# Kernel tuning notes

Measured on AMD Instinct MI355X. Metric: run time of the kernel, lower is better.

Reference implementation:

```python
import jax, jax.numpy as jnp
import numpy as np

N_EMBED = 768
N_HEAD = 12
HEAD = N_EMBED // N_HEAD
B, T = 4, 2048


def setup_inputs() -> dict:
    key = jax.random.key(0)
    ks = jax.random.split(key, 12)
    s = 0.02
    d = N_EMBED
    return {
        "x": jax.random.normal(ks[0], (B, T, d), jnp.float32),
        "ln1_g": jnp.ones((d,), jnp.float32),
        "ln1_b": jnp.zeros((d,), jnp.float32),
        "w_attn": jax.random.normal(ks[1], (d, 3 * d), jnp.float32) * s,
        "b_attn": jnp.zeros((3 * d,), jnp.float32),
        "w_aproj": jax.random.normal(ks[2], (d, d), jnp.float32) * s,
        "b_aproj": jnp.zeros((d,), jnp.float32),
        "ln2_g": jnp.ones((d,), jnp.float32),
        "ln2_b": jnp.zeros((d,), jnp.float32),
        "w_fc": jax.random.normal(ks[3], (d, 4 * d), jnp.float32) * s,
        "b_fc": jnp.zeros((4 * d,), jnp.float32),
        "w_mproj": jax.random.normal(ks[4], (4 * d, d), jnp.float32) * s,
        "b_mproj": jnp.zeros((d,), jnp.float32),
    }


def _layernorm(x, g, b, eps=1e-5):
    mu = jnp.mean(x, axis=-1, keepdims=True)
    var = jnp.var(x, axis=-1, keepdims=True)
    return (x - mu) * jax.lax.rsqrt(var + eps) * g + b


def _attn(x, w_attn, b_attn, w_aproj, b_aproj):
    Bq, Tq, C = x.shape
    qkv = x @ w_attn + b_attn  # [B,T,3C]
    q, k, v = jnp.split(qkv, 3, axis=2)
    q = q.reshape(Bq, Tq, N_HEAD, HEAD).transpose(0, 2, 1, 3)  # [B,H,T,hd]
    k = k.reshape(Bq, Tq, N_HEAD, HEAD).transpose(0, 2, 1, 3)
    v = v.reshape(Bq, Tq, N_HEAD, HEAD).transpose(0, 2, 1, 3)
    att = jnp.einsum("bhqd,bhkd->bhqk", q, k) * (1.0 / np.sqrt(HEAD))
    causal = jnp.tril(jnp.ones((Tq, Tq), bool))
    att = jnp.where(causal, att, -jnp.inf)
    att = jax.nn.softmax(att, axis=-1)
    y = jnp.einsum("bhqk,bhkd->bhqd", att, v)
    y = y.transpose(0, 2, 1, 3).reshape(Bq, Tq, C)
    return y @ w_aproj + b_aproj


def reference(x, ln1_g, ln1_b, w_attn, b_attn, w_aproj, b_aproj,
              ln2_g, ln2_b, w_fc, b_fc, w_mproj, b_mproj):
    x = x + _attn(_layernorm(x, ln1_g, ln1_b), w_attn, b_attn, w_aproj, b_aproj)
    h = _layernorm(x, ln2_g, ln2_b)
    h = jax.nn.gelu(h @ w_fc + b_fc, approximate=False)
    x = x + (h @ w_mproj + b_mproj)
    return x
```

## Files before the change

### kernel.cpp

```cpp
#include <hip/hip_runtime.h>
#include <hip/hip_bf16.h>

#define NE 768
#define NH 12
#define HD 64
#define BB 4
#define TT 2048
#define ROWS (BB*TT)

typedef __attribute__((ext_vector_type(8))) short bf16x8;
typedef __attribute__((ext_vector_type(4))) float f32x4;

#define WAITV(N) asm volatile("s_waitcnt vmcnt(" #N ")" ::: "memory")
#define BARSYNC()                                   \
  do {                                              \
    __builtin_amdgcn_sched_barrier(0);              \
    __builtin_amdgcn_s_barrier();                   \
    __builtin_amdgcn_sched_barrier(0);              \
  } while (0)

__device__ __forceinline__ short f2bf(float f) {
  __hip_bfloat16 h = __float2bfloat16(f);
  union { __hip_bfloat16 h; short s; } u; u.h = h; return u.s;
}

__device__ __forceinline__ void gload16(const void* g, void* l) {
  __builtin_amdgcn_global_load_lds(
      (const __attribute__((address_space(1))) void*)g,
      (__attribute__((address_space(3))) void*)l,
      16, 0, 0);
}

__device__ __forceinline__ void xcd_remap(int id, int nbn, int& bm, int& bn) {
  int x = id & 7;
  int j = id >> 3;
  bm = x * 8 + j / nbn;
  bn = j % nbn;
}

__global__ __launch_bounds__(256) void wtrans_kernel(
    const float* __restrict__ W, short* __restrict__ Wt, int K, int N) {
  __shared__ short tile[64 * 65];
  int k0 = blockIdx.x * 64, n0 = blockIdx.y * 64;
  int t = threadIdx.x;
#pragma unroll
  for (int p = 0; p < 16; ++p) {
    int idx = p * 256 + t;
    int r = idx >> 6, c = idx & 63;
    tile[r * 65 + c] = f2bf(W[(size_t)(k0 + r) * N + n0 + c]);
  }
  __syncthreads();
#pragma unroll
  for (int p = 0; p < 16; ++p) {
    int idx = p * 256 + t;
    int rr = idx >> 6, cc = idx & 63;
    Wt[(size_t)(n0 + rr) * K + k0 + cc] = tile[cc * 65 + rr];
  }
}

__global__ __launch_bounds__(256) void vtrans_kernel(
    const short* __restrict__ qkv, short* __restrict__ vt) {
  __shared__ short tile[64 * 65];
  int bh = blockIdx.x;
  int b = bh / NH, h = bh % NH;
  int t0 = blockIdx.y * 64;
  int t = threadIdx.x;
#pragma unroll
  for (int p = 0; p < 16; ++p) {
    int idx = p * 256 + t;
    int r = idx >> 6, c = idx & 63;
    tile[r * 65 + c] =
        qkv[(size_t)(b * TT + t0 + r) * (3 * NE) + 2 * NE + h * HD + c];
  }
  __syncthreads();
#pragma unroll
  for (int p = 0; p < 16; ++p) {
    int idx = p * 256 + t;
    int rr = idx >> 6, cc = idx & 63;
    vt[(size_t)bh * HD * TT + (size_t)rr * TT + t0 + cc] = tile[cc * 65 + rr];
  }
}

__global__ __launch_bounds__(64) void ln_kernel(
    const float* __restrict__ x, const float* __restrict__ g,
    const float* __restrict__ b, short* __restrict__ out) {
  int row = blockIdx.x, l = threadIdx.x;
  const float* xr = x + (size_t)row * NE;
  float4 v[3];
  float s = 0.f, ss = 0.f;
#pragma unroll
  for (int i = 0; i < 3; ++i) {
    v[i] = *reinterpret_cast<const float4*>(xr + l * 4 + i * 256);
    s += v[i].x + v[i].y + v[i].z + v[i].w;
    ss += v[i].x * v[i].x + v[i].y * v[i].y + v[i].z * v[i].z + v[i].w * v[i].w;
  }
#pragma unroll
  for (int m = 1; m < 64; m <<= 1) {
    s += __shfl_xor(s, m);
    ss += __shfl_xor(ss, m);
  }
  float mu = s * (1.0f / NE);
  float var = ss * (1.0f / NE) - mu * mu;
  float rstd = rsqrtf(var + 1e-5f);
#pragma unroll
  for (int i = 0; i < 3; ++i) {
    float4 gv = *reinterpret_cast<const float4*>(g + l * 4 + i * 256);
    float4 bv = *reinterpret_cast<const float4*>(b + l * 4 + i * 256);
    short4 o;
    o.x = f2bf((v[i].x - mu) * rstd * gv.x + bv.x);
    o.y = f2bf((v[i].y - mu) * rstd * gv.y + bv.y);
    o.z = f2bf((v[i].z - mu) * rstd * gv.z + bv.z);
    o.w = f2bf((v[i].w - mu) * rstd * gv.w + bv.w);
    *reinterpret_cast<short4*>(out + (size_t)row * NE + l * 4 + i * 256) = o;
  }
}

template <int EPI>
__global__ __launch_bounds__(256) void gemm_kernel(
    const short* __restrict__ A, const short* __restrict__ Bt,
    const float* __restrict__ bias, const float* __restrict__ resid,
    void* __restrict__ Cout, int M, int N, int K, int nbn) {
  __shared__ short As[3][128 * 32];
  __shared__ short Bs[3][128 * 32];
  int t = threadIdx.x;
  int w = t >> 6, l = t & 63;
  int wr = w >> 1, wc = w & 1;
  int bm, bn;
  xcd_remap(blockIdx.x, nbn, bm, bn);
  int lr = l & 15, g4 = l >> 4;

  f32x4 acc[4][4];
#pragma unroll
  for (int i = 0; i < 4; ++i)
#pragma unroll
    for (int j = 0; j < 4; ++j) acc[i][j] = (f32x4){0.f, 0.f, 0.f, 0.f};

  int r0 = t >> 2;
  int cs = ((t & 3) ^ (r0 & 3)) * 8;
  const short* ga = A + (size_t)(bm * 128) * K;
  const short* gb = Bt + (size_t)(bn * 128) * K;

#pragma unroll
  for (int p = 0; p < 2; ++p) {
    int ko = p * 32;
    gload16(ga + (size_t)r0 * K + ko + cs, &As[p][t * 8]);
    gload16(ga + (size_t)(r0 + 64) * K + ko + cs, &As[p][(t + 256) * 8]);
    gload16(gb + (size_t)r0 * K + ko + cs, &Bs[p][t * 8]);
    gload16(gb + (size_t)(r0 + 64) * K + ko + cs, &Bs[p][(t + 256) * 8]);
  }

  int xorA = (lr & 3) << 4;
  int nk = K >> 5;
  int cur = 0, prv = 2;
  for (int kt = 0; kt < nk; ++kt) {
    if (kt < nk - 1) WAITV(4); else WAITV(0);
    BARSYNC();
    if (kt + 2 < nk) {
      int ko = (kt + 2) * 32;
      gload16(ga + (size_t)r0 * K + ko + cs, &As[prv][t * 8]);
      gload16(ga + (size_t)(r0 + 64) * K + ko + cs, &As[prv][(t + 256) * 8]);
      gload16(gb + (size_t)r0 * K + ko + cs, &Bs[prv][t * 8]);
      gload16(gb + (size_t)(r0 + 64) * K + ko + cs, &Bs[prv][(t + 256) * 8]);
    }
    __builtin_amdgcn_sched_barrier(0);
    const char* Ab = (const char*)As[cur];
    const char* Bb = (const char*)Bs[cur];
    bf16x8 af[4], bfr[4];
#pragma unroll
    for (int i = 0; i < 4; ++i)
      af[i] = *reinterpret_cast<const bf16x8*>(
          Ab + (((wr * 64 + i * 16 + lr) * 64 + g4 * 16) ^ xorA));
#pragma unroll
    for (int j = 0; j < 4; ++j)
      bfr[j] = *reinterpret_cast<const bf16x8*>(
          Bb + (((wc * 64 + j * 16 + lr) * 64 + g4 * 16) ^ xorA));
#pragma unroll
    for (int i = 0; i < 4; ++i)
#pragma unroll
      for (int j = 0; j < 4; ++j)
        acc[i][j] = __builtin_amdgcn_mfma_f32_16x16x32_bf16(af[i], bfr[j], acc[i][j], 0, 0, 0);
    prv = cur;
    cur = (cur == 2) ? 0 : cur + 1;
  }

  int rbase = bm * 128 + wr * 64;
  int cbase = bn * 128 + wc * 64;
#pragma unroll
  for (int i = 0; i < 4; ++i) {
#pragma unroll
    for (int r = 0; r < 4; ++r) {
      int row = rbase + i * 16 + g4 * 4 + r;
#pragma unroll
      for (int j = 0; j < 4; ++j) {
        int col = cbase + j * 16 + lr;
        float v = acc[i][j][r] + bias[col];
        if (EPI == 0) {
          ((short*)Cout)[(size_t)row * N + col] = f2bf(v);
        } else if (EPI == 1) {
          v = 0.5f * v * (1.0f + erff(v * 0.70710678118654752f));
          ((short*)Cout)[(size_t)row * N + col] = f2bf(v);
        } else {
          ((float*)Cout)[(size_t)row * N + col] = v + resid[(size_t)row * N + col];
        }
      }
    }
  }
}

template <int EPI>
__global__ __launch_bounds__(256) void gemm64_kernel(
    const short* __restrict__ A, const short* __restrict__ Bt,
    const float* __restrict__ bias, const float* __restrict__ resid,
    void* __restrict__ Cout, int M, int N, int K, int nbn) {
  __shared__ short As[4][128 * 32];
  __shared__ short Bs[4][64 * 32];
  int t = threadIdx.x;
  int w = t >> 6, l = t & 63;
  int bm, bn;
  xcd_remap(blockIdx.x, nbn, bm, bn);
  int lr = l & 15, g4 = l >> 4;

  f32x4 acc[2][4];
#pragma unroll
  for (int i = 0; i < 2; ++i)
#pragma unroll
    for (int j = 0; j < 4; ++j) acc[i][j] = (f32x4){0.f, 0.f, 0.f, 0.f};

  int r0 = t >> 2;
  int cs = ((t & 3) ^ (r0 & 3)) * 8;
  const short* ga = A + (size_t)(bm * 128) * K;
  const short* gb = Bt + (size_t)(bn * 64) * K;

#pragma unroll
  for (int p = 0; p < 3; ++p) {
    int ko = p * 32;
    gload16(ga + (size_t)r0 * K + ko + cs, &As[p][t * 8]);
    gload16(ga + (size_t)(r0 + 64) * K + ko + cs, &As[p][(t + 256) * 8]);
    gload16(gb + (size_t)r0 * K + ko + cs, &Bs[p][t * 8]);
  }

  int xorA = (lr & 3) << 4;
  int nk = K >> 5;
  for (int kt = 0; kt < nk; ++kt) {
    int bi = kt & 3;
    int rem = nk - 1 - kt;
    if (rem >= 2) WAITV(6);
    else if (rem == 1) WAITV(3);
    else WAITV(0);
    BARSYNC();
    if (kt + 3 < nk) {
      int ko = (kt + 3) * 32;
      int nb = (kt + 3) & 3;
      gload16(ga + (size_t)r0 * K + ko + cs, &As[nb][t * 8]);
      gload16(ga + (size_t)(r0 + 64) * K + ko + cs, &As[nb][(t + 256) * 8]);
      gload16(gb + (size_t)r0 * K + ko + cs, &Bs[nb][t * 8]);
    }
    __builtin_amdgcn_sched_barrier(0);
    const char* Ab = (const char*)As[bi];
    const char* Bb = (const char*)Bs[bi];
    bf16x8 af[2], bfr[4];
#pragma unroll
    for (int i = 0; i < 2; ++i)
      af[i] = *reinterpret_cast<const bf16x8*>(
          Ab + (((w * 32 + i * 16 + lr) * 64 + g4 * 16) ^ xorA));
#pragma unroll
    for (int j = 0; j < 4; ++j)
      bfr[j] = *reinterpret_cast<const bf16x8*>(
          Bb + (((j * 16 + lr) * 64 + g4 * 16) ^ xorA));
#pragma unroll
    for (int i = 0; i < 2; ++i)
#pragma unroll
      for (int j = 0; j < 4; ++j)
        acc[i][j] = __builtin_amdgcn_mfma_f32_16x16x32_bf16(af[i], bfr[j], acc[i][j], 0, 0, 0);
  }

  int rbase = bm * 128 + w * 32;
  int cbase = bn * 64;
#pragma unroll
  for (int i = 0; i < 2; ++i) {
#pragma unroll
    for (int r = 0; r < 4; ++r) {
      int row = rbase + i * 16 + g4 * 4 + r;
#pragma unroll
      for (int j = 0; j < 4; ++j) {
        int col = cbase + j * 16 + lr;
        float v = acc[i][j][r] + bias[col];
        if (EPI == 0) {
          ((short*)Cout)[(size_t)row * N + col] = f2bf(v);
        } else if (EPI == 1) {
          v = 0.5f * v * (1.0f + erff(v * 0.70710678118654752f));
          ((short*)Cout)[(size_t)row * N + col] = f2bf(v);
        } else {
          ((float*)Cout)[(size_t)row * N + col] = v + resid[(size_t)row * N + col];
        }
      }
    }
  }
}

__global__ __launch_bounds__(256, 4) void attn_kernel(
    const short* __restrict__ qkv, const short* __restrict__ vt,
    short* __restrict__ y) {
  __shared__ short Ks[2][64 * 64];
  __shared__ short Vs[2][64 * 64];
  int t = threadIdx.x, w = t >> 6, l = t & 63;
  int lr = l & 15, g = l >> 4, lkb = g * 8;
  int bh = blockIdx.x;
  int b = bh / NH, h = bh % NH;
  int qt = ((int)gridDim.y - 1) - blockIdx.y;
  int qbase = qt * 64;
  const int rstride = 3 * NE;

  const short* qrow = qkv + (size_t)(b * TT + qbase + w * 16 + lr) * rstride + h * HD + lkb;
  bf16x8 qf0 = *reinterpret_cast<const bf16x8*>(qrow);
  bf16x8 qf1 = *reinterpret_cast<const bf16x8*>(qrow + 32);

  f32x4 o[4];
#pragma unroll
  for (int j = 0; j < 4; ++j) o[j] = (f32x4){0.f, 0.f, 0.f, 0.f};
  float m_run = -3e38f, l_run = 0.f;

  int ci0 = t, ci1 = t + 256;
  int row0 = ci0 >> 3, c0 = ((ci0 & 7) ^ (row0 & 7)) * 8;
  int row1 = ci1 >> 3, c1 = ((ci1 & 7) ^ (row1 & 7)) * 8;

  const short* kbase = qkv + (size_t)(b * TT) * rstride + NE + h * HD;
  const short* vtb = vt + (size_t)bh * HD * TT;

  gload16(kbase + (size_t)row0 * rstride + c0, &Ks[0][ci0 * 8]);
  gload16(kbase + (size_t)row1 * rstride + c1, &Ks[0][ci1 * 8]);
  gload16(vtb + (size_t)row0 * TT + c0, &Vs[0][ci0 * 8]);
  gload16(vtb + (size_t)row1 * TT + c1, &Vs[0][ci1 * 8]);

  int qmin = qbase + w * 16;
  int srcA = ((g & 1) * 2) * 16 + lr;
  int srcB = srcA + 16;
  bool ghi = (g >= 2);

  int nkv = qt + 1;
  for (int kt = 0; kt < nkv; ++kt) {
    int bi = kt & 1;
    int kvbase = kt * 64;
    bool pre = (kt + 1 < nkv);
    __syncthreads();

    if (pre) {
      int nb = kvbase + 64;
      gload16(kbase + (size_t)(nb + row0) * rstride + c0, &Ks[bi ^ 1][ci0 * 8]);
      gload16(kbase + (size_t)(nb + row1) * rstride + c1, &Ks[bi ^ 1][ci1 * 8]);
      gload16(vtb + (size_t)row0 * TT + nb + c0, &Vs[bi ^ 1][ci0 * 8]);
      gload16(vtb + (size_t)row1 * TT + nb + c1, &Vs[bi ^ 1][ci1 * 8]);
    }

    f32x4 s[4];
#pragma unroll
    for (int nt = 0; nt < 4; ++nt) {
      int row = nt * 16 + lr;
      bf16x8 kf0 = *reinterpret_cast<const bf16x8*>(
          (char*)Ks[bi] + ((row * 128 + lkb * 2) ^ ((lr & 7) << 4)));
      bf16x8 kf1 = *reinterpret_cast<const bf16x8*>(
          (char*)Ks[bi] + ((row * 128 + 64 + lkb * 2) ^ ((lr & 7) << 4)));
      f32x4 st = (f32x4){0.f, 0.f, 0.f, 0.f};
      st = __builtin_amdgcn_mfma_f32_16x16x32_bf16(kf0, qf0, st, 0, 0, 0);
      st = __builtin_amdgcn_mfma_f32_16x16x32_bf16(kf1, qf1, st, 0, 0, 0);
      s[nt] = st;
    }

    if (kvbase + 63 > qmin) {
      int qabs = qmin + lr;
#pragma unroll
      for (int nt = 0; nt < 4; ++nt)
#pragma unroll
        for (int r = 0; r < 4; ++r) {
          int kp = kvbase + nt * 16 + g * 4 + r;
          s[nt][r] = (kp <= qabs) ? s[nt][r] * 0.125f : -3e38f;
        }
    } else {
#pragma unroll
      for (int nt = 0; nt < 4; ++nt)
#pragma unroll
        for (int r = 0; r < 4; ++r)
          s[nt][r] *= 0.125f;
    }

    float mx = s[0][0];
#pragma unroll
    for (int nt = 0; nt < 4; ++nt)
#pragma unroll
      for (int r = 0; r < 4; ++r) mx = fmaxf(mx, s[nt][r]);
    mx = fmaxf(mx, __shfl_xor(mx, 16));
    mx = fmaxf(mx, __shfl_xor(mx, 32));
    if (__any(mx > m_run + 8.f)) {
      float mn = fmaxf(m_run, mx);
      float al = __expf(m_run - mn);
      m_run = mn;
      l_run *= al;
      float al0 = __shfl(al, g * 4 + 0);
      float al1 = __shfl(al, g * 4 + 1);
      float al2 = __shfl(al, g * 4 + 2);
      float al3 = __shfl(al, g * 4 + 3);
#pragma unroll
      for (int j = 0; j < 4; ++j) {
        o[j][0] *= al0; o[j][1] *= al1; o[j][2] *= al2; o[j][3] *= al3;
      }
    }
    float rs = 0.f;
#pragma unroll
    for (int nt = 0; nt < 4; ++nt)
#pragma unroll
      for (int r = 0; r < 4; ++r) {
        float p = __expf(s[nt][r] - m_run);
        s[nt][r] = p;
        rs += p;
      }
    rs += __shfl_xor(rs, 16);
    rs += __shfl_xor(rs, 32);
    l_run += rs;

    unsigned int pw[4][2];
#pragma unroll
    for (int nt = 0; nt < 4; ++nt)
#pragma unroll
      for (int pr = 0; pr < 2; ++pr)
        pw[nt][pr] = (unsigned int)(unsigned short)f2bf(s[nt][2 * pr]) |
                     ((unsigned int)(unsigned short)f2bf(s[nt][2 * pr + 1]) << 16);

#pragma unroll
    for (int c = 0; c < 2; ++c) {
      unsigned int a00 = __shfl(pw[c * 2 + 0][0], srcA);
      unsigned int a01 = __shfl(pw[c * 2 + 0][1], srcA);
      unsigned int a02 = __shfl(pw[c * 2 + 0][0], srcB);
      unsigned int a03 = __shfl(pw[c * 2 + 0][1], srcB);
      unsigned int a10 = __shfl(pw[c * 2 + 1][0], srcA);
      unsigned int a11 = __shfl(pw[c * 2 + 1][1], srcA);
      unsigned int a12 = __shfl(pw[c * 2 + 1][0], srcB);
      unsigned int a13 = __shfl(pw[c * 2 + 1][1], srcB);
      unsigned int u0 = ghi ? a10 : a00;
      unsigned int u1 = ghi ? a11 : a01;
      unsigned int u2 = ghi ? a12 : a02;
      unsigned int u3 = ghi ? a13 : a03;
      bf16x8 pa;
      pa[0] = (short)(u0 & 0xffffu); pa[1] = (short)(u0 >> 16);
      pa[2] = (short)(u1 & 0xffffu); pa[3] = (short)(u1 >> 16);
      pa[4] = (short)(u2 & 0xffffu); pa[5] = (short)(u2 >> 16);
      pa[6] = (short)(u3 & 0xffffu); pa[7] = (short)(u3 >> 16);
#pragma unroll
      for (int j = 0; j < 4; ++j) {
        int vrow = j * 16 + lr;
        bf16x8 vf = *reinterpret_cast<const bf16x8*>(
            (char*)Vs[bi] + ((vrow * 128 + c * 64 + lkb * 2) ^ ((lr & 7) << 4)));
        o[j] = __builtin_amdgcn_mfma_f32_16x16x32_bf16(pa, vf, o[j], 0, 0, 0);
      }
    }
  }

  float inv = 1.0f / l_run;
  float i0 = __shfl(inv, g * 4 + 0);
  float i1 = __shfl(inv, g * 4 + 1);
  float i2 = __shfl(inv, g * 4 + 2);
  float i3 = __shfl(inv, g * 4 + 3);
#pragma unroll
  for (int r = 0; r < 4; ++r) {
    float ir = (r == 0) ? i0 : (r == 1) ? i1 : (r == 2) ? i2 : i3;
    size_t row = (size_t)(b * TT + qbase + w * 16 + g * 4 + r);
#pragma unroll
    for (int j = 0; j < 4; ++j)
      y[row * NE + h * HD + j * 16 + lr] = f2bf(o[j][r] * ir);
  }
}

extern "C" void kernel_launch(void* const* d_in, const int* in_sizes, int n_in,
                              void* d_out, int out_size, void* d_ws, size_t ws_size,
                              hipStream_t stream) {
  (void)in_sizes; (void)n_in; (void)out_size; (void)ws_size;
  const float* x       = (const float*)d_in[0];
  const float* ln1_g   = (const float*)d_in[1];
  const float* ln1_b   = (const float*)d_in[2];
  const float* w_attn  = (const float*)d_in[3];
  const float* b_attn  = (const float*)d_in[4];
  const float* w_aproj = (const float*)d_in[5];
  const float* b_aproj = (const float*)d_in[6];
  const float* ln2_g   = (const float*)d_in[7];
  const float* ln2_b   = (const float*)d_in[8];
  const float* w_fc    = (const float*)d_in[9];
  const float* b_fc    = (const float*)d_in[10];
  const float* w_mproj = (const float*)d_in[11];
  const float* b_mproj = (const float*)d_in[12];

  char* ws = (char*)d_ws;
  size_t off = 0;
  auto alloc = [&](size_t bytes) {
    char* p = ws + off;
    off += (bytes + 255) & ~(size_t)255;
    return p;
  };
  short* wt_attn  = (short*)alloc((size_t)2304 * 768 * 2);
  short* wt_aproj = (short*)alloc((size_t)768 * 768 * 2);
  short* wt_fc    = (short*)alloc((size_t)3072 * 768 * 2);
  short* wt_mproj = (short*)alloc((size_t)768 * 3072 * 2);
  short* lnb  = (short*)alloc((size_t)ROWS * 768 * 2);
  short* qkvb = (short*)alloc((size_t)ROWS * 3072 * 2);
  short* yb   = (short*)alloc((size_t)ROWS * 768 * 2);
  float* x2   = (float*)alloc((size_t)ROWS * 768 * 4);
  short* vtg = lnb;

  wtrans_kernel<<<dim3(768 / 64, 2304 / 64), 256, 0, stream>>>(w_attn, wt_attn, 768, 2304);
  wtrans_kernel<<<dim3(768 / 64, 768 / 64), 256, 0, stream>>>(w_aproj, wt_aproj, 768, 768);
  wtrans_kernel<<<dim3(768 / 64, 3072 / 64), 256, 0, stream>>>(w_fc, wt_fc, 768, 3072);
  wtrans_kernel<<<dim3(3072 / 64, 768 / 64), 256, 0, stream>>>(w_mproj, wt_mproj, 3072, 768);

  ln_kernel<<<ROWS, 64, 0, stream>>>(x, ln1_g, ln1_b, lnb);
  gemm_kernel<0><<<64 * 18, 256, 0, stream>>>(
      lnb, wt_attn, b_attn, nullptr, qkvb, ROWS, 2304, 768, 18);
  vtrans_kernel<<<dim3(BB * NH, TT / 64), 256, 0, stream>>>(qkvb, vtg);
  attn_kernel<<<dim3(BB * NH, TT / 64), 256, 0, stream>>>(qkvb, vtg, yb);
  gemm64_kernel<2><<<64 * 12, 256, 0, stream>>>(
      yb, wt_aproj, b_aproj, x, x2, ROWS, 768, 768, 12);
  ln_kernel<<<ROWS, 64, 0, stream>>>(x2, ln2_g, ln2_b, lnb);
  gemm_kernel<1><<<64 * 24, 256, 0, stream>>>(
      lnb, wt_fc, b_fc, nullptr, qkvb, ROWS, 3072, 768, 24);
  gemm64_kernel<2><<<64 * 12, 256, 0, stream>>>(
      qkvb, wt_mproj, b_mproj, x2, (float*)d_out, ROWS, 768, 3072, 12);
}
```

Baseline: 303.9 us.

## Fold softmax scale into QKV epilogue, use exp2, packed bf16 cvt, merge weight transposes

Multiplies the Q columns by 0.125·log2(e) in the QKV GEMM epilogue, so the attention kernel no longer scales the scores and can use raw v_exp_f32 (base-2) in place of __expf. The rescale threshold is adjusted to the base-2 domain. The probability conversion uses the packed v_cvt_pk_bf16_f32 instruction and a union in place of per-element packing. The four weight-transpose launches are merged into one kernel with a block-index dispatch. Rounding Q to bf16 after scaling changes numerics slightly.

```diff
diff --git a/kernel.cpp b/kernel.cpp
--- a/kernel.cpp
+++ b/kernel.cpp
@@ -7,6 +7,7 @@
 #define BB 4
 #define TT 2048
 #define ROWS (BB*TT)
+#define QSCALE 0.18033688011112042f
 
 typedef __attribute__((ext_vector_type(8))) short bf16x8;
 typedef __attribute__((ext_vector_type(4))) float f32x4;
@@ -24,6 +25,18 @@
   union { __hip_bfloat16 h; short s; } u; u.h = h; return u.s;
 }
 
+__device__ __forceinline__ float exp2fast(float x) {
+  float r;
+  asm("v_exp_f32 %0, %1" : "=v"(r) : "v"(x));
+  return r;
+}
+
+__device__ __forceinline__ unsigned int cvtpk(float lo, float hi) {
+  unsigned int r;
+  asm("v_cvt_pk_bf16_f32 %0, %1, %2" : "=v"(r) : "v"(lo), "v"(hi));
+  return r;
+}
+
 __device__ __forceinline__ void gload16(const void* g, void* l) {
   __builtin_amdgcn_global_load_lds(
       (const __attribute__((address_space(1))) void*)g,
@@ -38,10 +51,19 @@
   bn = j % nbn;
 }
 
-__global__ __launch_bounds__(256) void wtrans_kernel(
-    const float* __restrict__ W, short* __restrict__ Wt, int K, int N) {
+__global__ __launch_bounds__(256) void wtrans_all_kernel(
+    const float* __restrict__ w_attn, const float* __restrict__ w_aproj,
+    const float* __restrict__ w_fc, const float* __restrict__ w_mproj,
+    short* __restrict__ o_attn, short* __restrict__ o_aproj,
+    short* __restrict__ o_fc, short* __restrict__ o_mproj) {
   __shared__ short tile[64 * 65];
-  int k0 = blockIdx.x * 64, n0 = blockIdx.y * 64;
+  int id = blockIdx.x;
+  const float* W; short* Wt; int K, N, bx, by;
+  if (id < 432)       { W = w_attn;  Wt = o_attn;  K = 768;  N = 2304; bx = id % 12;  by = id / 12; }
+  else if (id < 576)  { id -= 432;  W = w_aproj; Wt = o_aproj; K = 768;  N = 768;  bx = id % 12;  by = id / 12; }
+  else if (id < 1152) { id -= 576;  W = w_fc;    Wt = o_fc;    K = 768;  N = 3072; bx = id % 12;  by = id / 12; }
+  else                { id -= 1152; W = w_mproj; Wt = o_mproj; K = 3072; N = 768;  bx = id % 48;  by = id / 48; }
+  int k0 = bx * 64, n0 = by * 64;
   int t = threadIdx.x;
 #pragma unroll
   for (int p = 0; p < 16; ++p) {
@@ -195,6 +217,7 @@
         int col = cbase + j * 16 + lr;
         float v = acc[i][j][r] + bias[col];
         if (EPI == 0) {
+          if (col < NE) v *= QSCALE;
           ((short*)Cout)[(size_t)row * N + col] = f2bf(v);
         } else if (EPI == 1) {
           v = 0.5f * v * (1.0f + erff(v * 0.70710678118654752f));
@@ -373,14 +396,8 @@
 #pragma unroll
         for (int r = 0; r < 4; ++r) {
           int kp = kvbase + nt * 16 + g * 4 + r;
-          s[nt][r] = (kp <= qabs) ? s[nt][r] * 0.125f : -3e38f;
+          s[nt][r] = (kp <= qabs) ? s[nt][r] : -3e38f;
         }
-    } else {
-#pragma unroll
-      for (int nt = 0; nt < 4; ++nt)
-#pragma unroll
-        for (int r = 0; r < 4; ++r)
-          s[nt][r] *= 0.125f;
     }
 
     float mx = s[0][0];
@@ -390,9 +407,9 @@
       for (int r = 0; r < 4; ++r) mx = fmaxf(mx, s[nt][r]);
     mx = fmaxf(mx, __shfl_xor(mx, 16));
     mx = fmaxf(mx, __shfl_xor(mx, 32));
-    if (__any(mx > m_run + 8.f)) {
+    if (__any(mx > m_run + 11.54f)) {
       float mn = fmaxf(m_run, mx);
-      float al = __expf(m_run - mn);
+      float al = exp2fast(m_run - mn);
       m_run = mn;
       l_run *= al;
       float al0 = __shfl(al, g * 4 + 0);
@@ -409,7 +426,7 @@
     for (int nt = 0; nt < 4; ++nt)
 #pragma unroll
       for (int r = 0; r < 4; ++r) {
-        float p = __expf(s[nt][r] - m_run);
+        float p = exp2fast(s[nt][r] - m_run);
         s[nt][r] = p;
         rs += p;
       }
@@ -422,8 +439,7 @@
     for (int nt = 0; nt < 4; ++nt)
 #pragma unroll
       for (int pr = 0; pr < 2; ++pr)
-        pw[nt][pr] = (unsigned int)(unsigned short)f2bf(s[nt][2 * pr]) |
-                     ((unsigned int)(unsigned short)f2bf(s[nt][2 * pr + 1]) << 16);
+        pw[nt][pr] = cvtpk(s[nt][2 * pr], s[nt][2 * pr + 1]);
 
 #pragma unroll
     for (int c = 0; c < 2; ++c) {
@@ -435,21 +451,17 @@
       unsigned int a11 = __shfl(pw[c * 2 + 1][1], srcA);
       unsigned int a12 = __shfl(pw[c * 2 + 1][0], srcB);
       unsigned int a13 = __shfl(pw[c * 2 + 1][1], srcB);
-      unsigned int u0 = ghi ? a10 : a00;
-      unsigned int u1 = ghi ? a11 : a01;
-      unsigned int u2 = ghi ? a12 : a02;
-      unsigned int u3 = ghi ? a13 : a03;
-      bf16x8 pa;
-      pa[0] = (short)(u0 & 0xffffu); pa[1] = (short)(u0 >> 16);
-      pa[2] = (short)(u1 & 0xffffu); pa[3] = (short)(u1 >> 16);
-      pa[4] = (short)(u2 & 0xffffu); pa[5] = (short)(u2 >> 16);
-      pa[6] = (short)(u3 & 0xffffu); pa[7] = (short)(u3 >> 16);
+      union { unsigned int u[4]; bf16x8 v; } pau;
+      pau.u[0] = ghi ? a10 : a00;
+      pau.u[1] = ghi ? a11 : a01;
+      pau.u[2] = ghi ? a12 : a02;
+      pau.u[3] = ghi ? a13 : a03;
 #pragma unroll
       for (int j = 0; j < 4; ++j) {
         int vrow = j * 16 + lr;
         bf16x8 vf = *reinterpret_cast<const bf16x8*>(
             (char*)Vs[bi] + ((vrow * 128 + c * 64 + lkb * 2) ^ ((lr & 7) << 4)));
-        o[j] = __builtin_amdgcn_mfma_f32_16x16x32_bf16(pa, vf, o[j], 0, 0, 0);
+        o[j] = __builtin_amdgcn_mfma_f32_16x16x32_bf16(pau.v, vf, o[j], 0, 0, 0);
       }
     }
   }
@@ -504,10 +516,8 @@
   float* x2   = (float*)alloc((size_t)ROWS * 768 * 4);
   short* vtg = lnb;
 
-  wtrans_kernel<<<dim3(768 / 64, 2304 / 64), 256, 0, stream>>>(w_attn, wt_attn, 768, 2304);
-  wtrans_kernel<<<dim3(768 / 64, 768 / 64), 256, 0, stream>>>(w_aproj, wt_aproj, 768, 768);
-  wtrans_kernel<<<dim3(768 / 64, 3072 / 64), 256, 0, stream>>>(w_fc, wt_fc, 768, 3072);
-  wtrans_kernel<<<dim3(3072 / 64, 768 / 64), 256, 0, stream>>>(w_mproj, wt_mproj, 3072, 768);
+  wtrans_all_kernel<<<1728, 256, 0, stream>>>(
+      w_attn, w_aproj, w_fc, w_mproj, wt_attn, wt_aproj, wt_fc, wt_mproj);
 
   ln_kernel<<<ROWS, 64, 0, stream>>>(x, ln1_g, ln1_b, lnb);
   gemm_kernel<0><<<64 * 18, 256, 0, stream>>>(
```

Result: faster. 290.3 us (-4.5%).
